# Optimization experiments

Measured on AMD Instinct MI355X. Metric: run time of the kernel, lower is better.

## Reference

```python
import jax, jax.numpy as jnp
import numpy as np

D, NA, K, R, C = 2048, 18, 64, 10, 10
H = NA * K  # worker LSTM hidden size = n_actions * k = 1152


def _lstm_cell(x, h, c, Wih, Whh, bih, bhh):
    # torch.nn.LSTMCell gate order: i, f, g, o
    gi, gf, gg, go = jnp.split(Wih @ x + bih + Whh @ h + bhh, 4)
    c2 = jax.nn.sigmoid(gf) * c + jax.nn.sigmoid(gi) * jnp.tanh(gg)
    h2 = jax.nn.sigmoid(go) * jnp.tanh(c2)
    return h2, c2


def setup_inputs() -> dict:
    key = jax.random.key(0)
    ks = jax.random.split(key, 25)
    def n(k, shape, s=0.05):
        return jax.random.normal(k, shape, jnp.float32) * s
    return {
        'x': n(ks[0], (2,), 1.0),
        'Wp': n(ks[1], (D, 2)), 'bp': n(ks[2], (D,)),
        'Wms': n(ks[3], (D, D)), 'bms': n(ks[4], (D,)),
        'Wih_m': n(ks[5], (4 * D, D)), 'Whh_m': n(ks[6], (4 * D, D)),
        'bih_m': n(ks[7], (4 * D,)), 'bhh_m': n(ks[8], (4 * D,)),
        'hn_m': n(ks[9], (R, D)), 'cn_m': n(ks[10], (R, D)),
        'Wmv': n(ks[11], (1, D)), 'bmv': n(ks[12], (1,)),
        'Wih_w': n(ks[13], (4 * H, D)), 'Whh_w': n(ks[14], (4 * H, H)),
        'bih_w': n(ks[15], (4 * H,)), 'bhh_w': n(ks[16], (4 * H,)),
        'hn_w': n(ks[17], (H,)), 'cn_w': n(ks[18], (H,)),
        'Wphi': n(ks[19], (K, D)),
        'Wc': n(ks[20], (1, H)), 'bc': n(ks[21], (1,)),
        'states': n(ks[22], (R + 1, D)), 'goals': n(ks[23], (R, D)),
        'tick': 3,
    }


def reference(x, Wp, bp, Wms, bms, Wih_m, Whh_m, bih_m, bhh_m, hn_m, cn_m,
              Wmv, bmv, Wih_w, Whh_w, bih_w, bhh_w, hn_w, cn_w, Wphi,
              Wc, bc, states, goals, tick):
    # percept (frozen): z = relu(Linear(2, d)(x)), used as detached data
    z = jax.lax.stop_gradient(jax.nn.relu(Wp @ x + bp))

    # ----- Manager -----
    s = jax.nn.relu(Wms @ z + bms)                       # f_mspace
    h_new, _ = _lstm_cell(s, hn_m[tick], cn_m[tick], Wih_m, Whh_m, bih_m, bhh_m)
    hn2 = hn_m.at[tick].set(h_new)                       # dLSTM tick buffer
    g_hat = hn2.sum(0) / R                               # mean over ring buffer
    g = g_hat / jnp.maximum(jnp.linalg.norm(g_hat), 1e-12)  # F.normalize(dim=0)
    m_value = Wmv @ g_hat + bmv
    g_det = jax.lax.stop_gradient(g)
    s_det = jax.lax.stop_gradient(s)

    # push into fixed-size lists (already at capacity -> pop front)
    goals2 = jnp.concatenate([goals[1:], g_det[None]], axis=0)    # (R, D)
    states2 = jnp.concatenate([states[1:], s_det[None]], axis=0)  # (R+1, D)

    # ----- Worker -----
    w = Wphi @ goals2.sum(0)                             # (K,)
    u_flat, _ = _lstm_cell(z, hn_w, cn_w, Wih_w, Whh_w, bih_w, bhh_w)
    logits = u_flat.reshape(NA, K) @ w                   # Categorical logits
    w_value = Wc @ u_flat + bc

    # ----- intrinsic reward (no-grad in original) -----
    cur = states2[-1]
    diffs = cur - states2[:-1]                           # (R, D)
    num = jnp.sum(diffs * goals2, axis=1)
    den = jnp.maximum(jnp.linalg.norm(diffs, axis=1), 1e-8) * \
          jnp.maximum(jnp.linalg.norm(goals2, axis=1), 1e-8)
    cos = num / den                                      # (R,)
    # original adds scalar cosine onto a (d,)-zeros vector then sums -> factor D
    w_intrinsic_reward = jax.lax.stop_gradient(D * jnp.sum(cos) / C)

    return logits, w_intrinsic_reward, w_value, m_value
```

## Files before the change

kernel.cpp:

```cpp
#include <hip/hip_runtime.h>
#include <math.h>

#define DD 2048
#define HH 1152
#define NAA 18
#define KK 64
#define RR 10

__device__ __forceinline__ float wred(float v) {
#pragma unroll
  for (int off = 32; off > 0; off >>= 1) v += __shfl_down(v, off);
  return v;
}

__device__ __forceinline__ float sigf(float x) { return 1.f / (1.f + expf(-x)); }

__global__ void k_s(const float* __restrict__ x, const float* __restrict__ Wp,
                    const float* __restrict__ bp, const float* __restrict__ Wms,
                    const float* __restrict__ bms, float* __restrict__ s_out,
                    float* __restrict__ scal) {
  __shared__ float z[DD];
  const float x0 = x[0], x1 = x[1];
  for (int i = threadIdx.x; i < DD; i += blockDim.x) {
    float v = fmaf(Wp[2 * i], x0, fmaf(Wp[2 * i + 1], x1, bp[i]));
    z[i] = fmaxf(v, 0.f);
  }
  if (blockIdx.x == 0 && threadIdx.x < 32) scal[threadIdx.x] = 0.f;
  __syncthreads();
  const int lane = threadIdx.x & 63;
  const int gw = blockIdx.x * (blockDim.x >> 6) + (threadIdx.x >> 6);
  const int nw = gridDim.x * (blockDim.x >> 6);
  for (int row = gw; row < DD; row += nw) {
    const float4* wr = (const float4*)(Wms + (size_t)row * DD);
    float acc = 0.f;
#pragma unroll
    for (int it = 0; it < 8; ++it) {
      float4 w4 = wr[it * 64 + lane];
      float4 z4 = *(const float4*)&z[4 * (it * 64 + lane)];
      acc = fmaf(w4.x, z4.x, acc); acc = fmaf(w4.y, z4.y, acc);
      acc = fmaf(w4.z, z4.z, acc); acc = fmaf(w4.w, z4.w, acc);
    }
    acc = wred(acc);
    if (lane == 0) s_out[row] = fmaxf(acc + bms[row], 0.f);
  }
}

__global__ void k_gates(const float* __restrict__ x, const float* __restrict__ Wp,
                        const float* __restrict__ bp, const float* __restrict__ s_in,
                        const int* __restrict__ tick,
                        const float* __restrict__ Wih_m, const float* __restrict__ Whh_m,
                        const float* __restrict__ bih_m, const float* __restrict__ bhh_m,
                        const float* __restrict__ hn_m,
                        const float* __restrict__ Wih_w, const float* __restrict__ Whh_w,
                        const float* __restrict__ bih_w, const float* __restrict__ bhh_w,
                        const float* __restrict__ hn_w,
                        float* __restrict__ gates_m, float* __restrict__ gates_w) {
  __shared__ float sv[DD];
  __shared__ float zv[DD];
  __shared__ float hm[DD];
  __shared__ float hw[HH];
  const int tk = *tick;
  const float x0 = x[0], x1 = x[1];
  for (int i = threadIdx.x; i < DD; i += blockDim.x) {
    sv[i] = s_in[i];
    float v = fmaf(Wp[2 * i], x0, fmaf(Wp[2 * i + 1], x1, bp[i]));
    zv[i] = fmaxf(v, 0.f);
    hm[i] = hn_m[tk * DD + i];
  }
  for (int i = threadIdx.x; i < HH; i += blockDim.x) hw[i] = hn_w[i];
  __syncthreads();
  const int lane = threadIdx.x & 63;
  const int gw = blockIdx.x * (blockDim.x >> 6) + (threadIdx.x >> 6);
  const int nw = gridDim.x * (blockDim.x >> 6);
  const int nrows = 4 * DD + 4 * HH;
  for (int row = gw; row < nrows; row += nw) {
    if (row < 4 * DD) {
      const float4* a = (const float4*)(Wih_m + (size_t)row * DD);
      const float4* b = (const float4*)(Whh_m + (size_t)row * DD);
      float acc = 0.f;
#pragma unroll
      for (int it = 0; it < 8; ++it) {
        float4 a4 = a[it * 64 + lane];
        float4 s4 = *(const float4*)&sv[4 * (it * 64 + lane)];
        acc = fmaf(a4.x, s4.x, acc); acc = fmaf(a4.y, s4.y, acc);
        acc = fmaf(a4.z, s4.z, acc); acc = fmaf(a4.w, s4.w, acc);
        float4 b4 = b[it * 64 + lane];
        float4 h4 = *(const float4*)&hm[4 * (it * 64 + lane)];
        acc = fmaf(b4.x, h4.x, acc); acc = fmaf(b4.y, h4.y, acc);
        acc = fmaf(b4.z, h4.z, acc); acc = fmaf(b4.w, h4.w, acc);
      }
      acc = wred(acc);
      if (lane == 0) gates_m[row] = acc + bih_m[row] + bhh_m[row];
    } else {
      const int j = row - 4 * DD;
      const float4* a = (const float4*)(Wih_w + (size_t)j * DD);
      float acc = 0.f;
#pragma unroll
      for (int it = 0; it < 8; ++it) {
        float4 a4 = a[it * 64 + lane];
        float4 z4 = *(const float4*)&zv[4 * (it * 64 + lane)];
        acc = fmaf(a4.x, z4.x, acc); acc = fmaf(a4.y, z4.y, acc);
        acc = fmaf(a4.z, z4.z, acc); acc = fmaf(a4.w, z4.w, acc);
      }
      const float4* b = (const float4*)(Whh_w + (size_t)j * HH);
#pragma unroll
      for (int it = 0; it < 4; ++it) {
        float4 b4 = b[it * 64 + lane];
        float4 h4 = *(const float4*)&hw[4 * (it * 64 + lane)];
        acc = fmaf(b4.x, h4.x, acc); acc = fmaf(b4.y, h4.y, acc);
        acc = fmaf(b4.z, h4.z, acc); acc = fmaf(b4.w, h4.w, acc);
      }
      if (lane < 32) {
        float4 b4 = b[256 + lane];
        float4 h4 = *(const float4*)&hw[4 * (256 + lane)];
        acc = fmaf(b4.x, h4.x, acc); acc = fmaf(b4.y, h4.y, acc);
        acc = fmaf(b4.z, h4.z, acc); acc = fmaf(b4.w, h4.w, acc);
      }
      acc = wred(acc);
      if (lane == 0) gates_w[j] = acc + bih_w[j] + bhh_w[j];
    }
  }
}

__global__ void k_cell(const float* __restrict__ gates_m, const float* __restrict__ gates_w,
                       const int* __restrict__ tick, const float* __restrict__ hn_m,
                       const float* __restrict__ cn_m, const float* __restrict__ cn_w,
                       const float* __restrict__ Wmv, const float* __restrict__ Wc,
                       const float* __restrict__ goals, const float* __restrict__ states,
                       const float* __restrict__ s_in,
                       float* __restrict__ g_hat, float* __restrict__ goalsA,
                       float* __restrict__ u_flat, float* __restrict__ scal) {
  const int t = blockIdx.x * blockDim.x + threadIdx.x;
  const int tk = *tick;
  float r_norm2 = 0.f, r_mval = 0.f, r_wval = 0.f, r_num9h = 0.f;
  float r_dd2[10], r_num[9], r_gg2[9];
#pragma unroll
  for (int r = 0; r < 10; ++r) r_dd2[r] = 0.f;
#pragma unroll
  for (int r = 0; r < 9; ++r) { r_num[r] = 0.f; r_gg2[r] = 0.f; }

  if (t < DD) {
    const int d = t;
    float gi = gates_m[d], gf = gates_m[DD + d], gg = gates_m[2 * DD + d], go = gates_m[3 * DD + d];
    float c = cn_m[tk * DD + d];
    float c2 = sigf(gf) * c + sigf(gi) * tanhf(gg);
    float hnew = sigf(go) * tanhf(c2);
    float sum = hnew;
#pragma unroll
    for (int r = 0; r < RR; ++r) sum += (r == tk) ? 0.f : hn_m[r * DD + d];
    float gh = sum * (1.f / RR);
    g_hat[d] = gh;
    r_norm2 = gh * gh;
    r_mval = Wmv[d] * gh;
    float ga = 0.f;
    float sd = s_in[d];
#pragma unroll
    for (int r = 0; r < RR; ++r) {
      float diff = sd - states[(r + 1) * DD + d];
      r_dd2[r] = diff * diff;
      if (r < 9) {
        float gl = goals[(r + 1) * DD + d];
        ga += gl;
        r_num[r] = diff * gl;
        r_gg2[r] = gl * gl;
      } else {
        r_num9h = diff * gh;
      }
    }
    goalsA[d] = ga;
  } else if (t < DD + HH) {
    const int j = t - DD;
    float gi = gates_w[j], gf = gates_w[HH + j], gg = gates_w[2 * HH + j], go = gates_w[3 * HH + j];
    float c = cn_w[j];
    float c2 = sigf(gf) * c + sigf(gi) * tanhf(gg);
    float u = sigf(go) * tanhf(c2);
    u_flat[j] = u;
    r_wval = Wc[j] * u;
  }

  r_norm2 = wred(r_norm2); r_mval = wred(r_mval);
  r_wval = wred(r_wval);   r_num9h = wred(r_num9h);
#pragma unroll
  for (int r = 0; r < 10; ++r) r_dd2[r] = wred(r_dd2[r]);
#pragma unroll
  for (int r = 0; r < 9; ++r) { r_num[r] = wred(r_num[r]); r_gg2[r] = wred(r_gg2[r]); }
  if ((threadIdx.x & 63) == 0) {
    atomicAdd(&scal[0], r_norm2);
    atomicAdd(&scal[1], r_mval);
    atomicAdd(&scal[2], r_wval);
    atomicAdd(&scal[3], r_num9h);
#pragma unroll
    for (int r = 0; r < 10; ++r) atomicAdd(&scal[4 + r], r_dd2[r]);
#pragma unroll
    for (int r = 0; r < 9; ++r) {
      atomicAdd(&scal[14 + r], r_num[r]);
      atomicAdd(&scal[23 + r], r_gg2[r]);
    }
  }
}

__global__ void k_w(const float* __restrict__ Wphi, const float* __restrict__ g_hat,
                    const float* __restrict__ goalsA, const float* __restrict__ scal,
                    float* __restrict__ wv) {
  __shared__ float vsum[DD];
  const float rn = 1.f / fmaxf(sqrtf(scal[0]), 1e-12f);
  for (int i = threadIdx.x; i < DD; i += blockDim.x)
    vsum[i] = fmaf(g_hat[i], rn, goalsA[i]);
  __syncthreads();
  const int lane = threadIdx.x & 63;
  const int gw = blockIdx.x * (blockDim.x >> 6) + (threadIdx.x >> 6);
  if (gw < KK) {
    const float4* a = (const float4*)(Wphi + (size_t)gw * DD);
    float acc = 0.f;
#pragma unroll
    for (int it = 0; it < 8; ++it) {
      float4 a4 = a[it * 64 + lane];
      float4 v4 = *(const float4*)&vsum[4 * (it * 64 + lane)];
      acc = fmaf(a4.x, v4.x, acc); acc = fmaf(a4.y, v4.y, acc);
      acc = fmaf(a4.z, v4.z, acc); acc = fmaf(a4.w, v4.w, acc);
    }
    acc = wred(acc);
    if (lane == 0) wv[gw] = acc;
  }
}

__global__ void k_final(const float* __restrict__ u_flat, const float* __restrict__ wv,
                        const float* __restrict__ scal, const float* __restrict__ bmv,
                        const float* __restrict__ bc, float* __restrict__ out) {
  __shared__ float wl[KK];
  if (threadIdx.x < KK) wl[threadIdx.x] = wv[threadIdx.x];
  __syncthreads();
  const int lane = threadIdx.x & 63;
  const int wid = threadIdx.x >> 6;
  const int nw = blockDim.x >> 6;
  for (int a = wid; a < NAA; a += nw) {
    float acc = u_flat[a * KK + lane] * wl[lane];
    acc = wred(acc);
    if (lane == 0) out[a] = acc;
  }
  if (threadIdx.x == 0) {
    float nrm = sqrtf(scal[0]);
    float rn = 1.f / fmaxf(nrm, 1e-12f);
    float gnorm = nrm * rn;
    float csum = 0.f;
    for (int r = 0; r < 9; ++r) {
      float den = fmaxf(sqrtf(scal[4 + r]), 1e-8f) * fmaxf(sqrtf(scal[23 + r]), 1e-8f);
      csum += scal[14 + r] / den;
    }
    float den9 = fmaxf(sqrtf(scal[13]), 1e-8f) * fmaxf(gnorm, 1e-8f);
    csum += (scal[3] * rn) / den9;
    out[NAA] = (float)DD * csum / 10.f;
    out[NAA + 1] = scal[2] + bc[0];
    out[NAA + 2] = scal[1] + bmv[0];
  }
}

extern "C" void kernel_launch(void* const* d_in, const int* in_sizes, int n_in,
                              void* d_out, int out_size, void* d_ws, size_t ws_size,
                              hipStream_t stream) {
  const float* x      = (const float*)d_in[0];
  const float* Wp     = (const float*)d_in[1];
  const float* bp     = (const float*)d_in[2];
  const float* Wms    = (const float*)d_in[3];
  const float* bms    = (const float*)d_in[4];
  const float* Wih_m  = (const float*)d_in[5];
  const float* Whh_m  = (const float*)d_in[6];
  const float* bih_m  = (const float*)d_in[7];
  const float* bhh_m  = (const float*)d_in[8];
  const float* hn_m   = (const float*)d_in[9];
  const float* cn_m   = (const float*)d_in[10];
  const float* Wmv    = (const float*)d_in[11];
  const float* bmv    = (const float*)d_in[12];
  const float* Wih_w  = (const float*)d_in[13];
  const float* Whh_w  = (const float*)d_in[14];
  const float* bih_w  = (const float*)d_in[15];
  const float* bhh_w  = (const float*)d_in[16];
  const float* hn_w   = (const float*)d_in[17];
  const float* cn_w   = (const float*)d_in[18];
  const float* Wphi   = (const float*)d_in[19];
  const float* Wc     = (const float*)d_in[20];
  const float* bc     = (const float*)d_in[21];
  const float* states = (const float*)d_in[22];
  const float* goals  = (const float*)d_in[23];
  const int*   tick   = (const int*)d_in[24];

  float* ws      = (float*)d_ws;
  float* gates_m = ws;
  float* gates_w = ws + 8192;
  float* s_buf   = ws + 12800;
  float* g_hat   = ws + 14848;
  float* goalsA  = ws + 16896;
  float* u_flat  = ws + 18944;
  float* wvec    = ws + 20096;
  float* scal    = ws + 20160;
  float* out     = (float*)d_out;

  hipLaunchKernelGGL(k_s, dim3(256), dim3(256), 0, stream,
                     x, Wp, bp, Wms, bms, s_buf, scal);
  hipLaunchKernelGGL(k_gates, dim3(640), dim3(256), 0, stream,
                     x, Wp, bp, s_buf, tick,
                     Wih_m, Whh_m, bih_m, bhh_m, hn_m,
                     Wih_w, Whh_w, bih_w, bhh_w, hn_w,
                     gates_m, gates_w);
  hipLaunchKernelGGL(k_cell, dim3(13), dim3(256), 0, stream,
                     gates_m, gates_w, tick, hn_m, cn_m, cn_w, Wmv, Wc,
                     goals, states, s_buf, g_hat, goalsA, u_flat, scal);
  hipLaunchKernelGGL(k_w, dim3(16), dim3(256), 0, stream,
                     Wphi, g_hat, goalsA, scal, wvec);
  hipLaunchKernelGGL(k_final, dim3(1), dim3(512), 0, stream,
                     u_flat, wvec, scal, bmv, bc, out);
}
```

Measured before the change: 291.2 us.

## Split gate GEMV into worker and manager kernels with one row per wave and batched loads

The combined gates kernel is split into a worker-gates kernel that runs first (it does not depend on s) and a manager-gates kernel that runs after s. Every kernel now assigns exactly one row per wavefront, with launch grids sized to match. All weight float4 loads for a row are issued into registers before any FMA, which raises memory-level parallelism for this bandwidth-bound GEMV. The cost is an extra kernel launch, more shared-memory fill work because there are many more blocks, and higher register pressure under launch_bounds(256,4).

```diff
diff --git a/kernel.cpp b/kernel.cpp
--- a/kernel.cpp
+++ b/kernel.cpp
@@ -15,10 +15,59 @@
 
 __device__ __forceinline__ float sigf(float x) { return 1.f / (1.f + expf(-x)); }
 
-__global__ void k_s(const float* __restrict__ x, const float* __restrict__ Wp,
-                    const float* __restrict__ bp, const float* __restrict__ Wms,
-                    const float* __restrict__ bms, float* __restrict__ s_out,
-                    float* __restrict__ scal) {
+__global__ __launch_bounds__(256, 4) void k_wg(
+    const float* __restrict__ x, const float* __restrict__ Wp,
+    const float* __restrict__ bp,
+    const float* __restrict__ Wih_w, const float* __restrict__ Whh_w,
+    const float* __restrict__ bih_w, const float* __restrict__ bhh_w,
+    const float* __restrict__ hn_w, float* __restrict__ gates_w) {
+  __shared__ float zv[DD];
+  __shared__ float hw[HH];
+  const float x0 = x[0], x1 = x[1];
+  for (int i = threadIdx.x; i < DD; i += blockDim.x) {
+    float v = fmaf(Wp[2 * i], x0, fmaf(Wp[2 * i + 1], x1, bp[i]));
+    zv[i] = fmaxf(v, 0.f);
+  }
+  for (int i = threadIdx.x; i < HH; i += blockDim.x) hw[i] = hn_w[i];
+  __syncthreads();
+  const int lane = threadIdx.x & 63;
+  const int row = blockIdx.x * (blockDim.x >> 6) + (threadIdx.x >> 6);
+  if (row >= 4 * HH) return;
+  const float4* a = (const float4*)(Wih_w + (size_t)row * DD);
+  const float4* b = (const float4*)(Whh_w + (size_t)row * HH);
+  float4 ra[8], rb[5];
+#pragma unroll
+  for (int it = 0; it < 8; ++it) ra[it] = a[it * 64 + lane];
+#pragma unroll
+  for (int it = 0; it < 4; ++it) rb[it] = b[it * 64 + lane];
+  rb[4] = (lane < 32) ? b[256 + lane] : make_float4(0.f, 0.f, 0.f, 0.f);
+  float acc = 0.f;
+#pragma unroll
+  for (int it = 0; it < 8; ++it) {
+    float4 z4 = *(const float4*)&zv[4 * (it * 64 + lane)];
+    acc = fmaf(ra[it].x, z4.x, acc); acc = fmaf(ra[it].y, z4.y, acc);
+    acc = fmaf(ra[it].z, z4.z, acc); acc = fmaf(ra[it].w, z4.w, acc);
+  }
+#pragma unroll
+  for (int it = 0; it < 4; ++it) {
+    float4 h4 = *(const float4*)&hw[4 * (it * 64 + lane)];
+    acc = fmaf(rb[it].x, h4.x, acc); acc = fmaf(rb[it].y, h4.y, acc);
+    acc = fmaf(rb[it].z, h4.z, acc); acc = fmaf(rb[it].w, h4.w, acc);
+  }
+  {
+    float4 h4 = *(const float4*)&hw[4 * (256 + (lane & 31))];
+    acc = fmaf(rb[4].x, h4.x, acc); acc = fmaf(rb[4].y, h4.y, acc);
+    acc = fmaf(rb[4].z, h4.z, acc); acc = fmaf(rb[4].w, h4.w, acc);
+  }
+  acc = wred(acc);
+  if (lane == 0) gates_w[row] = acc + bih_w[row] + bhh_w[row];
+}
+
+__global__ __launch_bounds__(256, 4) void k_s(
+    const float* __restrict__ x, const float* __restrict__ Wp,
+    const float* __restrict__ bp, const float* __restrict__ Wms,
+    const float* __restrict__ bms, float* __restrict__ s_out,
+    float* __restrict__ scal) {
   __shared__ float z[DD];
   const float x0 = x[0], x1 = x[1];
   for (int i = threadIdx.x; i < DD; i += blockDim.x) {
@@ -28,98 +77,61 @@
   if (blockIdx.x == 0 && threadIdx.x < 32) scal[threadIdx.x] = 0.f;
   __syncthreads();
   const int lane = threadIdx.x & 63;
-  const int gw = blockIdx.x * (blockDim.x >> 6) + (threadIdx.x >> 6);
-  const int nw = gridDim.x * (blockDim.x >> 6);
-  for (int row = gw; row < DD; row += nw) {
-    const float4* wr = (const float4*)(Wms + (size_t)row * DD);
-    float acc = 0.f;
-#pragma unroll
-    for (int it = 0; it < 8; ++it) {
-      float4 w4 = wr[it * 64 + lane];
-      float4 z4 = *(const float4*)&z[4 * (it * 64 + lane)];
-      acc = fmaf(w4.x, z4.x, acc); acc = fmaf(w4.y, z4.y, acc);
-      acc = fmaf(w4.z, z4.z, acc); acc = fmaf(w4.w, z4.w, acc);
-    }
-    acc = wred(acc);
-    if (lane == 0) s_out[row] = fmaxf(acc + bms[row], 0.f);
-  }
-}
-
-__global__ void k_gates(const float* __restrict__ x, const float* __restrict__ Wp,
-                        const float* __restrict__ bp, const float* __restrict__ s_in,
-                        const int* __restrict__ tick,
-                        const float* __restrict__ Wih_m, const float* __restrict__ Whh_m,
-                        const float* __restrict__ bih_m, const float* __restrict__ bhh_m,
-                        const float* __restrict__ hn_m,
-                        const float* __restrict__ Wih_w, const float* __restrict__ Whh_w,
-                        const float* __restrict__ bih_w, const float* __restrict__ bhh_w,
-                        const float* __restrict__ hn_w,
-                        float* __restrict__ gates_m, float* __restrict__ gates_w) {
+  const int row = blockIdx.x * (blockDim.x >> 6) + (threadIdx.x >> 6);
+  if (row >= DD) return;
+  const float4* wr = (const float4*)(Wms + (size_t)row * DD);
+  float4 rw[8];
+#pragma unroll
+  for (int it = 0; it < 8; ++it) rw[it] = wr[it * 64 + lane];
+  float acc = 0.f;
+#pragma unroll
+  for (int it = 0; it < 8; ++it) {
+    float4 z4 = *(const float4*)&z[4 * (it * 64 + lane)];
+    acc = fmaf(rw[it].x, z4.x, acc); acc = fmaf(rw[it].y, z4.y, acc);
+    acc = fmaf(rw[it].z, z4.z, acc); acc = fmaf(rw[it].w, z4.w, acc);
+  }
+  acc = wred(acc);
+  if (lane == 0) s_out[row] = fmaxf(acc + bms[row], 0.f);
+}
+
+__global__ __launch_bounds__(256, 4) void k_mg(
+    const float* __restrict__ s_in, const int* __restrict__ tick,
+    const float* __restrict__ Wih_m, const float* __restrict__ Whh_m,
+    const float* __restrict__ bih_m, const float* __restrict__ bhh_m,
+    const float* __restrict__ hn_m, float* __restrict__ gates_m) {
   __shared__ float sv[DD];
-  __shared__ float zv[DD];
   __shared__ float hm[DD];
-  __shared__ float hw[HH];
   const int tk = *tick;
-  const float x0 = x[0], x1 = x[1];
   for (int i = threadIdx.x; i < DD; i += blockDim.x) {
     sv[i] = s_in[i];
-    float v = fmaf(Wp[2 * i], x0, fmaf(Wp[2 * i + 1], x1, bp[i]));
-    zv[i] = fmaxf(v, 0.f);
     hm[i] = hn_m[tk * DD + i];
   }
-  for (int i = threadIdx.x; i < HH; i += blockDim.x) hw[i] = hn_w[i];
-  __syncthreads();
-  const int lane = threadIdx.x & 63;
-  const int gw = blockIdx.x * (blockDim.x >> 6) + (threadIdx.x >> 6);
-  const int nw = gridDim.x * (blockDim.x >> 6);
-  const int nrows = 4 * DD + 4 * HH;
-  for (int row = gw; row < nrows; row += nw) {
-    if (row < 4 * DD) {
-      const float4* a = (const float4*)(Wih_m + (size_t)row * DD);
-      const float4* b = (const float4*)(Whh_m + (size_t)row * DD);
-      float acc = 0.f;
-#pragma unroll
-      for (int it = 0; it < 8; ++it) {
-        float4 a4 = a[it * 64 + lane];
-        float4 s4 = *(const float4*)&sv[4 * (it * 64 + lane)];
-        acc = fmaf(a4.x, s4.x, acc); acc = fmaf(a4.y, s4.y, acc);
-        acc = fmaf(a4.z, s4.z, acc); acc = fmaf(a4.w, s4.w, acc);
-        float4 b4 = b[it * 64 + lane];
-        float4 h4 = *(const float4*)&hm[4 * (it * 64 + lane)];
-        acc = fmaf(b4.x, h4.x, acc); acc = fmaf(b4.y, h4.y, acc);
-        acc = fmaf(b4.z, h4.z, acc); acc = fmaf(b4.w, h4.w, acc);
-      }
-      acc = wred(acc);
-      if (lane == 0) gates_m[row] = acc + bih_m[row] + bhh_m[row];
-    } else {
-      const int j = row - 4 * DD;
-      const float4* a = (const float4*)(Wih_w + (size_t)j * DD);
-      float acc = 0.f;
-#pragma unroll
-      for (int it = 0; it < 8; ++it) {
-        float4 a4 = a[it * 64 + lane];
-        float4 z4 = *(const float4*)&zv[4 * (it * 64 + lane)];
-        acc = fmaf(a4.x, z4.x, acc); acc = fmaf(a4.y, z4.y, acc);
-        acc = fmaf(a4.z, z4.z, acc); acc = fmaf(a4.w, z4.w, acc);
-      }
-      const float4* b = (const float4*)(Whh_w + (size_t)j * HH);
-#pragma unroll
-      for (int it = 0; it < 4; ++it) {
-        float4 b4 = b[it * 64 + lane];
-        float4 h4 = *(const float4*)&hw[4 * (it * 64 + lane)];
-        acc = fmaf(b4.x, h4.x, acc); acc = fmaf(b4.y, h4.y, acc);
-        acc = fmaf(b4.z, h4.z, acc); acc = fmaf(b4.w, h4.w, acc);
-      }
-      if (lane < 32) {
-        float4 b4 = b[256 + lane];
-        float4 h4 = *(const float4*)&hw[4 * (256 + lane)];
-        acc = fmaf(b4.x, h4.x, acc); acc = fmaf(b4.y, h4.y, acc);
-        acc = fmaf(b4.z, h4.z, acc); acc = fmaf(b4.w, h4.w, acc);
-      }
-      acc = wred(acc);
-      if (lane == 0) gates_w[j] = acc + bih_w[j] + bhh_w[j];
-    }
-  }
+  __syncthreads();
+  const int lane = threadIdx.x & 63;
+  const int row = blockIdx.x * (blockDim.x >> 6) + (threadIdx.x >> 6);
+  if (row >= 4 * DD) return;
+  const float4* a = (const float4*)(Wih_m + (size_t)row * DD);
+  const float4* b = (const float4*)(Whh_m + (size_t)row * DD);
+  float4 ra[8], rb[8];
+#pragma unroll
+  for (int it = 0; it < 8; ++it) ra[it] = a[it * 64 + lane];
+#pragma unroll
+  for (int it = 0; it < 8; ++it) rb[it] = b[it * 64 + lane];
+  float acc = 0.f;
+#pragma unroll
+  for (int it = 0; it < 8; ++it) {
+    float4 s4 = *(const float4*)&sv[4 * (it * 64 + lane)];
+    acc = fmaf(ra[it].x, s4.x, acc); acc = fmaf(ra[it].y, s4.y, acc);
+    acc = fmaf(ra[it].z, s4.z, acc); acc = fmaf(ra[it].w, s4.w, acc);
+  }
+#pragma unroll
+  for (int it = 0; it < 8; ++it) {
+    float4 h4 = *(const float4*)&hm[4 * (it * 64 + lane)];
+    acc = fmaf(rb[it].x, h4.x, acc); acc = fmaf(rb[it].y, h4.y, acc);
+    acc = fmaf(rb[it].z, h4.z, acc); acc = fmaf(rb[it].w, h4.w, acc);
+  }
+  acc = wred(acc);
+  if (lane == 0) gates_m[row] = acc + bih_m[row] + bhh_m[row];
 }
 
 __global__ void k_cell(const float* __restrict__ gates_m, const float* __restrict__ gates_w,
@@ -211,13 +223,15 @@
   const int gw = blockIdx.x * (blockDim.x >> 6) + (threadIdx.x >> 6);
   if (gw < KK) {
     const float4* a = (const float4*)(Wphi + (size_t)gw * DD);
+    float4 rw[8];
+#pragma unroll
+    for (int it = 0; it < 8; ++it) rw[it] = a[it * 64 + lane];
     float acc = 0.f;
 #pragma unroll
     for (int it = 0; it < 8; ++it) {
-      float4 a4 = a[it * 64 + lane];
       float4 v4 = *(const float4*)&vsum[4 * (it * 64 + lane)];
-      acc = fmaf(a4.x, v4.x, acc); acc = fmaf(a4.y, v4.y, acc);
-      acc = fmaf(a4.z, v4.z, acc); acc = fmaf(a4.w, v4.w, acc);
+      acc = fmaf(rw[it].x, v4.x, acc); acc = fmaf(rw[it].y, v4.y, acc);
+      acc = fmaf(rw[it].z, v4.z, acc); acc = fmaf(rw[it].w, v4.w, acc);
     }
     acc = wred(acc);
     if (lane == 0) wv[gw] = acc;
@@ -295,13 +309,12 @@
   float* scal    = ws + 20160;
   float* out     = (float*)d_out;
 
-  hipLaunchKernelGGL(k_s, dim3(256), dim3(256), 0, stream,
+  hipLaunchKernelGGL(k_wg, dim3(1152), dim3(256), 0, stream,
+                     x, Wp, bp, Wih_w, Whh_w, bih_w, bhh_w, hn_w, gates_w);
+  hipLaunchKernelGGL(k_s, dim3(512), dim3(256), 0, stream,
                      x, Wp, bp, Wms, bms, s_buf, scal);
-  hipLaunchKernelGGL(k_gates, dim3(640), dim3(256), 0, stream,
-                     x, Wp, bp, s_buf, tick,
-                     Wih_m, Whh_m, bih_m, bhh_m, hn_m,
-                     Wih_w, Whh_w, bih_w, bhh_w, hn_w,
-                     gates_m, gates_w);
+  hipLaunchKernelGGL(k_mg, dim3(2048), dim3(256), 0, stream,
+                     s_buf, tick, Wih_m, Whh_m, bih_m, bhh_m, hn_m, gates_m);
   hipLaunchKernelGGL(k_cell, dim3(13), dim3(256), 0, stream,
                      gates_m, gates_w, tick, hn_m, cn_m, cn_w, Wmv, Wc,
                      goals, states, s_buf, g_hat, goalsA, u_flat, scal);
```

Result: no change. 288.5 us (-0.9%).
